# Kernel optimization log

Hardware: AMD Instinct MI355X
Metric: run time of the kernel (lower is better)

The kernel has to match this reference:

```python
import jax, jax.numpy as jnp
import numpy as np

B, CIN, H, W = 64, 3, 96, 96
COUT, KH, KW = 96, 5, 5
STRIDE, PAD = 2, 2
LR, K_TOP, DELTA, P_LEB = 0.02, 2, -0.4, 3.0
PREC = 1e-30


def im2col(x):
    # torch nn.Unfold ordering: channel-major (C, kh, kw) flattened -> [B, C*KH*KW, L]
    xp = jnp.pad(x, ((0, 0), (0, 0), (PAD, PAD), (PAD, PAD)))
    Hout = (H + 2 * PAD - KH) // STRIDE + 1
    Wout = (W + 2 * PAD - KW) // STRIDE + 1
    cols = []
    for i in range(KH):  # small fixed kernel loop (25 slices)
        for j in range(KW):
            cols.append(xp[:, :, i:i + STRIDE * (Hout - 1) + 1:STRIDE,
                           j:j + STRIDE * (Wout - 1) + 1:STRIDE])
    patches = jnp.stack(cols, axis=2)  # [B, C, KH*KW, Hout, Wout]
    return patches.reshape(x.shape[0], CIN * KH * KW, Hout * Wout)  # [B, K, L]


def setup_inputs() -> dict:
    key = jax.random.key(0)
    k1, k2 = jax.random.split(key)
    inp = jax.random.normal(k1, (B, CIN, H, W), dtype=jnp.float32)
    weight = jax.random.normal(k2, (COUT, CIN, KH, KW), dtype=jnp.float32)  # init.normal_
    return {"input": inp, "weight": weight}


def reference(input, weight):
    # standard conv forward (F.conv2d, no bias)
    out = jax.lax.conv_general_dilated(
        input, weight, (STRIDE, STRIDE), [(PAD, PAD), (PAD, PAD)],
        dimension_numbers=("NCHW", "OIHW", "NCHW"))

    # --- Krotov-Hopfield Hebbian update ---
    pre = im2col(input)                      # [B, K, L]
    Wm = weight.reshape(COUT, -1)            # [O, K]
    # sign(W) * |W|^(p-1) @ pre
    tot = jnp.einsum("ok,bkl->bol", jnp.sign(Wm) * jnp.abs(Wm) ** (P_LEB - 1.0), pre)  # [B,O,L]

    Bn, _, L = tot.shape
    _, idx = jax.lax.top_k(tot.transpose(0, 2, 1), K_TOP)   # [B, L, k] over output channels
    vals = jnp.concatenate([jnp.ones((1,), tot.dtype),
                            jnp.full((K_TOP - 1,), DELTA, tot.dtype)])  # top-1 -> 1.0, rest -> delta
    act = jnp.zeros((Bn, L, COUT), tot.dtype).at[
        jnp.arange(Bn)[:, None, None], jnp.arange(L)[None, :, None], idx
    ].set(jnp.broadcast_to(vals, (Bn, L, K_TOP)))
    act = act.transpose(0, 2, 1)             # [B, O, L]

    yx = jnp.einsum("bol,bkl->ok", act, pre) / L          # mean over L, sum over batch
    yy = (act * tot).sum(0).mean(1)                        # [O]
    ds = yx - yy[:, None] * Wm                             # [O, K]
    nc = jnp.maximum(jnp.max(jnp.abs(ds)), PREC)
    new_weight = weight + LR * (ds / nc).reshape(weight.shape)
    return out, new_weight
```

## Files before the change

### kernel.cpp

```cpp
#include <hip/hip_runtime.h>

#define B_     64
#define HW_    96
#define COUT_  96
#define KK_    75
#define KPAD   96
#define HOUT_  48
#define L_     2304
#define LR_    0.02f
#define DELTA_ -0.4f
#define OUT_ELEMS (B_*COUT_*L_)
#define XPITCH 100
#define XSLOTS 3368
#define C2     192
#define NPART  (B_*12)
#define ROW    (COUT_*KK_ + COUT_)
#define X2P    99
#define X2N    (33*X2P)
#define CTP    196

typedef __attribute__((ext_vector_type(8))) short short8v;
typedef __attribute__((ext_vector_type(4))) float float4v;
typedef __attribute__((ext_vector_type(4))) unsigned uint4v;

__device__ __forceinline__ unsigned short f2bf(float f) {
  unsigned u = __float_as_uint(f);
  u += 0x7fff + ((u >> 16) & 1);
  return (unsigned short)(u >> 16);
}

__device__ __forceinline__ void ins2(float v, int o, float& v1, int& o1,
                                     float& v2, int& o2) {
  bool b1 = (v > v1) || (v == v1 && o < o1);
  bool b2 = (v > v2) || (v == v2 && o < o2);
  if (b1)      { v2 = v1; o2 = o1; v1 = v; o1 = o; }
  else if (b2) { v2 = v;  o2 = o; }
}

__global__ __launch_bounds__(256) void k0_prep(const float* __restrict__ w,
                                               unsigned short* __restrict__ wbf) {
  int i = blockIdx.x * 256 + threadIdx.x;
  if (i >= 192 * KPAD) return;
  int row = i / KPAD, k = i - row * KPAD;
  float v = 0.0f;
  if (k < KK_) {
    float ww = w[(row % COUT_) * KK_ + k];
    v = (row < COUT_) ? ww : ww * fabsf(ww);
  }
  wbf[i] = f2bf(v);
}

__device__ __forceinline__ int wswz(int blk, int row) {
  return (blk < 8) ? (blk ^ (row & 7)) : (blk ^ (row & 3));
}

__global__ __launch_bounds__(256, 3) void k1_mfma(
    const float* __restrict__ x, const unsigned short* __restrict__ wbf,
    float* __restrict__ out, float4* __restrict__ top2)
{
  __shared__ __align__(16) char ldsRaw[50336];
  unsigned short* wlds = (unsigned short*)ldsRaw;
  float* xs = (float*)(ldsRaw + 36864);
  float* cT = (float*)ldsRaw;
  const int tid = threadIdx.x;
  const int lane = tid & 63, wq = tid >> 6;
  const int b = blockIdx.y;
  const int bx = blockIdx.x;
  const int col = lane & 15, g = lane >> 4;
  const float* xb = x + (size_t)b * (3 * HW_ * HW_);

  #pragma unroll
  for (int i = 0; i < 9; ++i) {
    int id = tid + i * 256;
    int row = id / 12, blk = id - row * 12;
    uint4v v = *(const uint4v*)(wbf + row * KPAD + blk * 8);
    *(uint4v*)((char*)wlds + row * 192 + wswz(blk, row) * 16) = v;
  }

  const int ihbase = 8 * bx - 2;
  #pragma unroll
  for (int i = 0; i < 14; ++i) {
    int idx = tid + i * 256;
    if (idx < XSLOTS) {
      int row = idx / XPITCH, iwr = idx - row * XPITCH;
      int c = row / 11, ihr = row - c * 11;
      int ih = ihbase + ihr, iw = iwr - 2;
      float v = 0.0f;
      if (c < 3 && (unsigned)ih < (unsigned)HW_ && (unsigned)iw < (unsigned)HW_)
        v = xb[(c * HW_ + ih) * HW_ + iw];
      xs[idx] = v;
    }
  }

  int offs[12][2];
  {
    const int base_fl = wq * 200 + 2 * col;
    #pragma unroll
    for (int kt = 0; kt < 3; ++kt)
      #pragma unroll
      for (int e2 = 0; e2 < 4; ++e2)
        #pragma unroll
        for (int par = 0; par < 2; ++par) {
          int k = kt * 32 + g * 8 + 2 * e2 + par;
          int c = k / 25, r = k - 25 * c, ki = r / 5, kj = r - 5 * ki;
          int fl = (k < KK_) ? base_fl + (c * 11 + ki) * XPITCH + kj
                             : 33 * XPITCH;
          offs[kt * 4 + e2][par] = fl * 4;
        }
  }

  __syncthreads();

  short8v bfr[3][3];
  #pragma unroll
  for (int nt = 0; nt < 3; ++nt)
    #pragma unroll
    for (int kt = 0; kt < 3; ++kt) {
      uint4v pk;
      #pragma unroll
      for (int e2 = 0; e2 < 4; ++e2) {
        const float* p0 = (const float*)((const char*)xs + offs[kt*4+e2][0]);
        const float* p1 = (const float*)((const char*)xs + offs[kt*4+e2][1]);
        float v0 = p0[nt * 32];
        float v1 = p1[nt * 32];
        pk[e2] = (unsigned)f2bf(v0) | ((unsigned)f2bf(v1) << 16);
      }
      bfr[nt][kt] = __builtin_bit_cast(short8v, pk);
    }

  const int lrow0 = (4 * bx + wq) * 48;
  float4v acc[3][6];

  #pragma unroll
  for (int nt = 0; nt < 3; ++nt)
    #pragma unroll
    for (int mt = 0; mt < 6; ++mt) acc[nt][mt] = (float4v)(0.0f);
  #pragma unroll
  for (int kt = 0; kt < 3; ++kt) {
    const int blk = kt * 4 + g;
    #pragma unroll
    for (int mt = 0; mt < 6; ++mt) {
      const int row = 96 + mt * 16 + col;
      short8v afr = *(const short8v*)(
          (const char*)wlds + row * 192 + wswz(blk, row) * 16);
      #pragma unroll
      for (int nt = 0; nt < 3; ++nt)
        acc[nt][mt] = __builtin_amdgcn_mfma_f32_16x16x32_bf16(
            afr, bfr[nt][kt], acc[nt][mt], 0, 0, 0);
    }
  }
  #pragma unroll
  for (int nt = 0; nt < 3; ++nt) {
    float v1 = -3.0e38f, v2 = -3.0e38f;
    int o1 = 0x7fffffff, o2 = 0x7fffffff;
    #pragma unroll
    for (int mt = 0; mt < 6; ++mt)
      #pragma unroll
      for (int r = 0; r < 4; ++r)
        ins2(acc[nt][mt][r], mt * 16 + g * 4 + r, v1, o1, v2, o2);
    #pragma unroll
    for (int st = 0; st < 2; ++st) {
      const int d = (st == 0) ? 16 : 32;
      float bv1 = __shfl_xor(v1, d, 64);
      int   bo1 = __shfl_xor(o1, d, 64);
      float bv2 = __shfl_xor(v2, d, 64);
      int   bo2 = __shfl_xor(o2, d, 64);
      ins2(bv1, bo1, v1, o1, v2, o2);
      ins2(bv2, bo2, v1, o1, v2, o2);
    }
    if (g == 0)
      top2[(size_t)b * L_ + lrow0 + nt * 16 + col] =
          make_float4(v1, __int_as_float(o1), v2, __int_as_float(o2));
  }

  #pragma unroll
  for (int nt = 0; nt < 3; ++nt)
    #pragma unroll
    for (int mt = 0; mt < 6; ++mt) acc[nt][mt] = (float4v)(0.0f);
  #pragma unroll
  for (int kt = 0; kt < 3; ++kt) {
    const int blk = kt * 4 + g;
    #pragma unroll
    for (int mt = 0; mt < 6; ++mt) {
      const int row = mt * 16 + col;
      short8v afr = *(const short8v*)(
          (const char*)wlds + row * 192 + wswz(blk, row) * 16);
      #pragma unroll
      for (int nt = 0; nt < 3; ++nt)
        acc[nt][mt] = __builtin_amdgcn_mfma_f32_16x16x32_bf16(
            afr, bfr[nt][kt], acc[nt][mt], 0, 0, 0);
    }
  }
  __syncthreads();

  const int blockl = bx * 192;
  #pragma unroll 1
  for (int h = 0; h < 2; ++h) {
    #pragma unroll
    for (int mt = 0; mt < 3; ++mt)
      #pragma unroll
      for (int r = 0; r < 4; ++r) {
        const int chl = mt * 16 + g * 4 + r;
        #pragma unroll
        for (int nt = 0; nt < 3; ++nt)
          cT[chl * CTP + wq * 48 + nt * 16 + col] = acc[nt][h * 3 + mt][r];
      }
    __syncthreads();
    const float4* cT4 = (const float4*)cT;
    #pragma unroll
    for (int i = 0; i < 9; ++i) {
      int idx = tid + i * 256;
      int ch = idx / 48, p4 = idx - ch * 48;
      float4 v = cT4[ch * (CTP / 4) + p4];
      *(float4*)&out[((size_t)b * COUT_ + h * 48 + ch) * L_ + blockl + 4 * p4] = v;
    }
    if (h == 0) __syncthreads();
  }
}

__global__ __launch_bounds__(256, 2) void k2_gemm(
    const float* __restrict__ x, const float4* __restrict__ top2,
    float* __restrict__ part)
{
  __shared__ __align__(16) unsigned short actS[COUT_ * C2];
  __shared__ __align__(16) unsigned short preT[COUT_ * C2];
  __shared__ __align__(16) unsigned short xsb[X2N + 13];
  __shared__ float yyS[COUT_];
  const int tid = threadIdx.x;
  const int b = blockIdx.y;
  const int bx = blockIdx.x;
  const int l0 = bx * C2;
  const float* xb = x + (size_t)b * (3 * HW_ * HW_);

  {
    float4* a4 = (float4*)actS;
    #pragma unroll
    for (int i = 0; i < 9; ++i) a4[tid + i * 256] = make_float4(0, 0, 0, 0);
    float4* p4 = (float4*)((char*)preT + KK_ * (C2 * 2));
    if (tid < 252) {
      p4[2 * tid]     = make_float4(0, 0, 0, 0);
      p4[2 * tid + 1] = make_float4(0, 0, 0, 0);
    }
    if (tid < COUT_) yyS[tid] = 0.0f;
  }

  const int ihb2 = 8 * bx - 2;
  #pragma unroll
  for (int i = 0; i < 13; ++i) {
    int idx = tid + i * 256;
    if (idx < X2N) {
      int row = idx / X2P, iwr = idx - row * X2P;
      int c = row / 11, ihr = row - c * 11;
      int ih = ihb2 + ihr, iw = iwr - 2;
      float v = 0.0f;
      if (c < 3 && (unsigned)ih < (unsigned)HW_ && (unsigned)iw < (unsigned)HW_)
        v = xb[(c * HW_ + ih) * HW_ + iw];
      xsb[idx] = f2bf(v);
    }
  }
  __syncthreads();

  if (tid < C2) {
    const int pos = tid;
    const int ohr = pos / HOUT_, ow = pos - ohr * HOUT_;
    const int pblk = pos >> 3, plo = (pos & 7) << 1;
    const unsigned short* xl = xsb + (2 * ohr) * X2P + 2 * ow;
    #pragma unroll
    for (int c = 0; c < 3; ++c)
      #pragma unroll
      for (int ki = 0; ki < 5; ++ki)
        #pragma unroll
        for (int kj = 0; kj < 5; ++kj) {
          int k = c * 25 + ki * 5 + kj;
          unsigned short v = xl[(c * 11 + ki) * X2P + kj];
          *(unsigned short*)((char*)preT +
              k * (C2 * 2) + ((pblk ^ (k & 7)) << 4) + plo) = v;
        }
    float4 t2 = top2[(size_t)b * L_ + l0 + pos];
    int o1 = __float_as_int(t2.y), o2 = __float_as_int(t2.w);
    *(unsigned short*)((char*)actS +
        o1 * (C2 * 2) + ((pblk ^ (o1 & 7)) << 4) + plo) = 0x3F80;
    *(unsigned short*)((char*)actS +
        o2 * (C2 * 2) + ((pblk ^ (o2 & 7)) << 4) + plo) = f2bf(DELTA_);
    atomicAdd(&yyS[o1], t2.x);
    atomicAdd(&yyS[o2], DELTA_ * t2.z);
  }
  __syncthreads();

  const int lane = tid & 63, w = tid >> 6;
  const int col = lane & 15, g = lane >> 4;
  const int mb = (w >> 1) * 48, nb = (w & 1) * 48;

  float4v acc[3][3];
  #pragma unroll
  for (int mt = 0; mt < 3; ++mt)
    #pragma unroll
    for (int nt = 0; nt < 3; ++nt) acc[mt][nt] = (float4v)(0.0f);

  #pragma unroll
  for (int kt = 0; kt < 6; ++kt) {
    short8v a[3], bf[3];
    #pragma unroll
    for (int mt = 0; mt < 3; ++mt) {
      int row = mb + mt * 16 + col;
      a[mt] = *(const short8v*)((char*)actS + row * (C2 * 2) +
                                (((kt * 4 + g) ^ (row & 7)) << 4));
    }
    #pragma unroll
    for (int nt = 0; nt < 3; ++nt) {
      int row = nb + nt * 16 + col;
      bf[nt] = *(const short8v*)((char*)preT + row * (C2 * 2) +
                                 (((kt * 4 + g) ^ (row & 7)) << 4));
    }
    #pragma unroll
    for (int mt = 0; mt < 3; ++mt)
      #pragma unroll
      for (int nt = 0; nt < 3; ++nt)
        acc[mt][nt] = __builtin_amdgcn_mfma_f32_16x16x32_bf16(
            a[mt], bf[nt], acc[mt][nt], 0, 0, 0);
  }
  __syncthreads();

  float* prow = part + (size_t)(b * 12 + bx) * ROW;
  #pragma unroll
  for (int mt = 0; mt < 3; ++mt)
    #pragma unroll
    for (int nt = 0; nt < 3; ++nt)
      #pragma unroll
      for (int r = 0; r < 4; ++r) {
        int m = mb + mt * 16 + g * 4 + r;
        int n = nb + nt * 16 + col;
        if (n < KK_) prow[m * KK_ + n] = acc[mt][nt][r];
      }
  if (tid < COUT_) prow[COUT_ * KK_ + tid] = yyS[tid];
}

__global__ __launch_bounds__(256) void k3a_reduce(
    const float* __restrict__ part, float* __restrict__ tmp)
{
  __shared__ float red[4][64];
  const int e = blockIdx.x * 64 + (threadIdx.x & 63);
  const int seg = threadIdx.x >> 6;
  const int p0 = blockIdx.y * 96 + seg * 24;
  float s = 0.0f;
  #pragma unroll 4
  for (int j = 0; j < 24; ++j) s += part[(size_t)(p0 + j) * ROW + e];
  red[seg][threadIdx.x & 63] = s;
  __syncthreads();
  if (seg == 0) {
    int ll = threadIdx.x & 63;
    tmp[(size_t)blockIdx.y * ROW + e] =
        (red[0][ll] + red[1][ll]) + (red[2][ll] + red[3][ll]);
  }
}

__global__ __launch_bounds__(256) void k3b_fold(
    const float* __restrict__ tmp, float* __restrict__ finals)
{
  int i = blockIdx.x * 256 + threadIdx.x;
  if (i >= ROW) return;
  float s = 0.0f;
  #pragma unroll
  for (int p = 0; p < 8; ++p) s += tmp[(size_t)p * ROW + i];
  finals[i] = s;
}

__global__ __launch_bounds__(256) void k4_finalize(
    const float* __restrict__ w, const float* __restrict__ finals,
    float* __restrict__ outw)
{
  __shared__ float dsS[COUT_ * KK_];
  __shared__ float wmax[4];
  __shared__ float ncS;
  const int tid = threadIdx.x;
  float m = 0.0f;
  for (int i = tid; i < COUT_ * KK_; i += 256) {
    int o = i / KK_;
    float d = finals[i] - finals[COUT_ * KK_ + o] * w[i];
    dsS[i] = d;
    m = fmaxf(m, fabsf(d));
  }
  #pragma unroll
  for (int s = 32; s > 0; s >>= 1) m = fmaxf(m, __shfl_xor(m, s, 64));
  if ((tid & 63) == 0) wmax[tid >> 6] = m;
  __syncthreads();
  if (tid == 0) {
    float n = fmaxf(fmaxf(wmax[0], wmax[1]), fmaxf(wmax[2], wmax[3]));
    ncS = fmaxf(n, 1e-30f);
  }
  __syncthreads();
  const float scale = LR_ / ncS;
  for (int i = tid; i < COUT_ * KK_; i += 256) {
    outw[i] = w[i] + scale * dsS[i];
  }
}

extern "C" void kernel_launch(void* const* d_in, const int* in_sizes, int n_in,
                              void* d_out, int out_size, void* d_ws, size_t ws_size,
                              hipStream_t stream) {
  (void)in_sizes; (void)n_in; (void)out_size; (void)ws_size;
  const float* x = (const float*)d_in[0];
  const float* w = (const float*)d_in[1];
  float* out  = (float*)d_out;
  float* outw = out + OUT_ELEMS;

  unsigned short* wbf = (unsigned short*)d_ws;
  float4* top2 = (float4*)((char*)d_ws + 192 * KPAD * 2);
  float*  part = (float*)((char*)top2 + (size_t)B_ * L_ * sizeof(float4));
  float*  finals = part + (size_t)NPART * ROW;
  float*  tmp    = finals + ROW;

  k0_prep   <<<dim3((192 * KPAD + 255) / 256), 256, 0, stream>>>(w, wbf);
  k1_mfma   <<<dim3(12, B_), 256, 0, stream>>>(x, wbf, out, top2);
  k2_gemm   <<<dim3(12, B_), 256, 0, stream>>>(x, top2, part);
  k3a_reduce<<<dim3(114, 8), 256, 0, stream>>>(part, tmp);
  k3b_fold  <<<dim3(29), 256, 0, stream>>>(tmp, finals);
  k4_finalize<<<dim3(1), 256, 0, stream>>>(w, finals, outw);
}
```

Before: 128.7 us.

## Compute conv output per 16-channel tile and stream through smaller LDS staging

The conv-output GEMM now runs one 16-channel M tile at a time and writes each tile straight through the LDS transpose buffer to global memory, instead of holding all six tiles (18 float4 accumulators) live. The transpose buffer now overlays the x staging area rather than the weight area, so the weights stay resident while tiles are computed. This cuts peak register pressure and may allow higher occupancy. In exchange it adds four more block-wide barriers per block and serialises MFMA work with the stores.

```diff
diff --git a/kernel.cpp b/kernel.cpp
--- a/kernel.cpp
+++ b/kernel.cpp
@@ -61,7 +61,7 @@
   __shared__ __align__(16) char ldsRaw[50336];
   unsigned short* wlds = (unsigned short*)ldsRaw;
   float* xs = (float*)(ldsRaw + 36864);
-  float* cT = (float*)ldsRaw;
+  float* cT = xs;
   const int tid = threadIdx.x;
   const int lane = tid & 63, wq = tid >> 6;
   const int b = blockIdx.y;
@@ -129,92 +129,86 @@
     }
 
   const int lrow0 = (4 * bx + wq) * 48;
-  float4v acc[3][6];
-
-  #pragma unroll
-  for (int nt = 0; nt < 3; ++nt)
-    #pragma unroll
-    for (int mt = 0; mt < 6; ++mt) acc[nt][mt] = (float4v)(0.0f);
-  #pragma unroll
-  for (int kt = 0; kt < 3; ++kt) {
-    const int blk = kt * 4 + g;
-    #pragma unroll
-    for (int mt = 0; mt < 6; ++mt) {
-      const int row = 96 + mt * 16 + col;
-      short8v afr = *(const short8v*)(
-          (const char*)wlds + row * 192 + wswz(blk, row) * 16);
-      #pragma unroll
-      for (int nt = 0; nt < 3; ++nt)
-        acc[nt][mt] = __builtin_amdgcn_mfma_f32_16x16x32_bf16(
-            afr, bfr[nt][kt], acc[nt][mt], 0, 0, 0);
-    }
-  }
-  #pragma unroll
-  for (int nt = 0; nt < 3; ++nt) {
-    float v1 = -3.0e38f, v2 = -3.0e38f;
-    int o1 = 0x7fffffff, o2 = 0x7fffffff;
-    #pragma unroll
-    for (int mt = 0; mt < 6; ++mt)
-      #pragma unroll
-      for (int r = 0; r < 4; ++r)
-        ins2(acc[nt][mt][r], mt * 16 + g * 4 + r, v1, o1, v2, o2);
-    #pragma unroll
-    for (int st = 0; st < 2; ++st) {
-      const int d = (st == 0) ? 16 : 32;
-      float bv1 = __shfl_xor(v1, d, 64);
-      int   bo1 = __shfl_xor(o1, d, 64);
-      float bv2 = __shfl_xor(v2, d, 64);
-      int   bo2 = __shfl_xor(o2, d, 64);
-      ins2(bv1, bo1, v1, o1, v2, o2);
-      ins2(bv2, bo2, v1, o1, v2, o2);
-    }
-    if (g == 0)
-      top2[(size_t)b * L_ + lrow0 + nt * 16 + col] =
-          make_float4(v1, __int_as_float(o1), v2, __int_as_float(o2));
-  }
-
-  #pragma unroll
-  for (int nt = 0; nt < 3; ++nt)
-    #pragma unroll
-    for (int mt = 0; mt < 6; ++mt) acc[nt][mt] = (float4v)(0.0f);
-  #pragma unroll
-  for (int kt = 0; kt < 3; ++kt) {
-    const int blk = kt * 4 + g;
-    #pragma unroll
-    for (int mt = 0; mt < 6; ++mt) {
+
+  {
+    float4v acc[3][6];
+    #pragma unroll
+    for (int nt = 0; nt < 3; ++nt)
+      #pragma unroll
+      for (int mt = 0; mt < 6; ++mt) acc[nt][mt] = (float4v)(0.0f);
+    #pragma unroll
+    for (int kt = 0; kt < 3; ++kt) {
+      const int blk = kt * 4 + g;
+      #pragma unroll
+      for (int mt = 0; mt < 6; ++mt) {
+        const int row = 96 + mt * 16 + col;
+        short8v afr = *(const short8v*)(
+            (const char*)wlds + row * 192 + wswz(blk, row) * 16);
+        #pragma unroll
+        for (int nt = 0; nt < 3; ++nt)
+          acc[nt][mt] = __builtin_amdgcn_mfma_f32_16x16x32_bf16(
+              afr, bfr[nt][kt], acc[nt][mt], 0, 0, 0);
+      }
+    }
+    #pragma unroll
+    for (int nt = 0; nt < 3; ++nt) {
+      float v1 = -3.0e38f, v2 = -3.0e38f;
+      int o1 = 0x7fffffff, o2 = 0x7fffffff;
+      #pragma unroll
+      for (int mt = 0; mt < 6; ++mt)
+        #pragma unroll
+        for (int r = 0; r < 4; ++r)
+          ins2(acc[nt][mt][r], mt * 16 + g * 4 + r, v1, o1, v2, o2);
+      #pragma unroll
+      for (int st = 0; st < 2; ++st) {
+        const int d = (st == 0) ? 16 : 32;
+        float bv1 = __shfl_xor(v1, d, 64);
+        int   bo1 = __shfl_xor(o1, d, 64);
+        float bv2 = __shfl_xor(v2, d, 64);
+        int   bo2 = __shfl_xor(o2, d, 64);
+        ins2(bv1, bo1, v1, o1, v2, o2);
+        ins2(bv2, bo2, v1, o1, v2, o2);
+      }
+      if (g == 0)
+        top2[(size_t)b * L_ + lrow0 + nt * 16 + col] =
+            make_float4(v1, __int_as_float(o1), v2, __int_as_float(o2));
+    }
+  }
+
+  __syncthreads();
+
+  const int blockl = bx * 192;
+  #pragma unroll 1
+  for (int mt = 0; mt < 6; ++mt) {
+    float4v a0 = (float4v)(0.0f), a1 = (float4v)(0.0f), a2 = (float4v)(0.0f);
+    #pragma unroll
+    for (int kt = 0; kt < 3; ++kt) {
+      const int blk = kt * 4 + g;
       const int row = mt * 16 + col;
       short8v afr = *(const short8v*)(
           (const char*)wlds + row * 192 + wswz(blk, row) * 16);
-      #pragma unroll
-      for (int nt = 0; nt < 3; ++nt)
-        acc[nt][mt] = __builtin_amdgcn_mfma_f32_16x16x32_bf16(
-            afr, bfr[nt][kt], acc[nt][mt], 0, 0, 0);
-    }
-  }
-  __syncthreads();
-
-  const int blockl = bx * 192;
-  #pragma unroll 1
-  for (int h = 0; h < 2; ++h) {
-    #pragma unroll
-    for (int mt = 0; mt < 3; ++mt)
-      #pragma unroll
-      for (int r = 0; r < 4; ++r) {
-        const int chl = mt * 16 + g * 4 + r;
-        #pragma unroll
-        for (int nt = 0; nt < 3; ++nt)
-          cT[chl * CTP + wq * 48 + nt * 16 + col] = acc[nt][h * 3 + mt][r];
-      }
+      a0 = __builtin_amdgcn_mfma_f32_16x16x32_bf16(afr, bfr[0][kt], a0, 0, 0, 0);
+      a1 = __builtin_amdgcn_mfma_f32_16x16x32_bf16(afr, bfr[1][kt], a1, 0, 0, 0);
+      a2 = __builtin_amdgcn_mfma_f32_16x16x32_bf16(afr, bfr[2][kt], a2, 0, 0, 0);
+    }
+    #pragma unroll
+    for (int r = 0; r < 4; ++r) {
+      const int chl = g * 4 + r;
+      float* cp = cT + chl * CTP + wq * 48 + col;
+      cp[0]  = a0[r];
+      cp[16] = a1[r];
+      cp[32] = a2[r];
+    }
     __syncthreads();
     const float4* cT4 = (const float4*)cT;
     #pragma unroll
-    for (int i = 0; i < 9; ++i) {
+    for (int i = 0; i < 3; ++i) {
       int idx = tid + i * 256;
       int ch = idx / 48, p4 = idx - ch * 48;
       float4 v = cT4[ch * (CTP / 4) + p4];
-      *(float4*)&out[((size_t)b * COUT_ + h * 48 + ch) * L_ + blockl + 4 * p4] = v;
-    }
-    if (h == 0) __syncthreads();
+      *(float4*)&out[((size_t)b * COUT_ + mt * 16 + ch) * L_ + blockl + 4 * p4] = v;
+    }
+    if (mt < 5) __syncthreads();
   }
 }
 
```

After: 111.0 us. 1.16x faster.
